# Performance work log

Measured on AMD Instinct MI355X. Metric: run time of the kernel, lower is better.

The kernel has to match this reference:

```python
import jax, jax.numpy as jnp
import numpy as np

KH, KW = 3, 3
STRIDE, PAD, DIL = 1, 1, 1


def setup_inputs() -> dict:
    key = jax.random.key(0)
    k1, k2, k3 = jax.random.split(key, 3)
    B, C, H, W, O = 8, 128, 64, 64, 128
    x = jax.random.normal(k1, (B, C, H, W), jnp.float32)
    # offset layout: [B, 2*K, Ho, Wo], pairs (dy, dx) per kernel tap
    offset = jax.random.normal(k2, (B, 2 * KH * KW, H, W), jnp.float32)
    n = C * KH * KW
    stdv = 1.0 / np.sqrt(n)
    weight = jax.random.uniform(k3, (O, C, KH, KW), jnp.float32, -stdv, stdv)
    bias = jnp.zeros((O,), jnp.float32)
    return {"x": x, "offset": offset, "weight": weight, "bias": bias}


def _deform_conv(x, offset, weight, bias):
    B, C, H, W = x.shape
    O = weight.shape[0]
    K = KH * KW
    Ho = (H + 2 * PAD - DIL * (KH - 1) - 1) // STRIDE + 1
    Wo = (W + 2 * PAD - DIL * (KW - 1) - 1) // STRIDE + 1

    off = offset.reshape(B, K, 2, Ho, Wo)  # (dy, dx) per tap

    # base sampling grid for each kernel tap: [K, Ho, Wo]
    hs = jnp.arange(Ho, dtype=jnp.float32) * STRIDE - PAD
    ws = jnp.arange(Wo, dtype=jnp.float32) * STRIDE - PAD
    ki = jnp.arange(KH, dtype=jnp.float32) * DIL
    kj = jnp.arange(KW, dtype=jnp.float32) * DIL
    base_y = (ki[:, None, None, None] + hs[None, None, :, None])  # [KH,1,Ho,1]
    base_x = (kj[None, :, None, None] + ws[None, None, None, :])  # [1,KW,1,Wo]
    base_y = jnp.broadcast_to(base_y, (KH, KW, Ho, Wo)).reshape(K, Ho, Wo)
    base_x = jnp.broadcast_to(base_x, (KH, KW, Ho, Wo)).reshape(K, Ho, Wo)

    py = base_y[None] + off[:, :, 0]  # [B,K,Ho,Wo]
    px = base_x[None] + off[:, :, 1]

    y0 = jnp.floor(py)
    x0 = jnp.floor(px)
    ly = py - y0  # fractional parts
    lx = px - x0
    y0i = y0.astype(jnp.int32)
    x0i = x0.astype(jnp.int32)

    flat = x.reshape(B, C, H * W)

    def gather(yi, xi, w):
        # zero outside the image (DCN zero-padding semantics)
        valid = (yi >= 0) & (yi < H) & (xi >= 0) & (xi < W)
        idx = jnp.clip(yi, 0, H - 1) * W + jnp.clip(xi, 0, W - 1)  # [B,K,Ho,Wo]
        g = jnp.take_along_axis(flat, idx.reshape(B, 1, -1), axis=2)
        g = g.reshape(B, C, K, Ho, Wo)
        wmask = (w * valid.astype(x.dtype))[:, None]  # [B,1,K,Ho,Wo]
        return g * wmask

    # bilinear accumulation over 4 corners -> im2col columns [B,C,K,Ho,Wo]
    cols = gather(y0i, x0i, (1 - ly) * (1 - lx))
    cols = cols + gather(y0i, x0i + 1, (1 - ly) * lx)
    cols = cols + gather(y0i + 1, x0i, ly * (1 - lx))
    cols = cols + gather(y0i + 1, x0i + 1, ly * lx)

    out = jnp.einsum('ock,bckhw->bohw', weight.reshape(O, C, K), cols)
    return out + bias[None, :, None, None]


def reference(x, offset, weight, bias):
    return _deform_conv(x, offset, weight, bias)
```

## Files before the change

### kernel.cpp

```cpp
#include <hip/hip_runtime.h>


#define BB 8
#define CC 128
#define HH 64
#define WW 64
#define OO 128
#define KTAPS 9

typedef __attribute__((ext_vector_type(8))) short bf16x8;
typedef __attribute__((ext_vector_type(4))) float f32x4;

__device__ __forceinline__ unsigned short f2bf(float f) {
    unsigned u = __float_as_uint(f);
    u += 0x7FFFu + ((u >> 16) & 1u);
    return (unsigned short)(u >> 16);
}
#if __has_builtin(__builtin_amdgcn_cvt_pk_bf16_f32)
typedef __attribute__((ext_vector_type(2))) __bf16 bf16x2_t;
__device__ __forceinline__ unsigned pack2bf(float lo, float hi) {
    bf16x2_t v = __builtin_amdgcn_cvt_pk_bf16_f32(lo, hi);
    unsigned r;
    __builtin_memcpy(&r, &v, 4);
    return r;
}
#else
__device__ __forceinline__ unsigned pack2bf(float lo, float hi) {
    return (unsigned)f2bf(lo) | ((unsigned)f2bf(hi) << 16);
}
#endif
__device__ __forceinline__ float bflo(unsigned p) { return __uint_as_float(p << 16); }
__device__ __forceinline__ float bfhi(unsigned p) { return __uint_as_float(p & 0xFFFF0000u); }

__global__ __launch_bounds__(256)
void prep_kernel(const float* __restrict__ x, const float* __restrict__ wgt,
                 unsigned short* __restrict__ xt, unsigned short* __restrict__ wpk) {
    const int t = threadIdx.x;
    if (blockIdx.x < 512) {
        __shared__ float tile[WW * 132];
        const int b = blockIdx.x >> 6;
        const int h = blockIdx.x & 63;
        const float* src = x + ((size_t)b * CC * HH + h) * WW;
        {
            const int wq = t & 15;
            const int cb = t >> 4;
#pragma unroll
            for (int it = 0; it < 8; ++it) {
                const int c = it * 16 + cb;
                const float4 v = *reinterpret_cast<const float4*>(src + (size_t)c * (HH * WW) + wq * 4);
                tile[(wq * 4 + 0) * 132 + c] = v.x;
                tile[(wq * 4 + 1) * 132 + c] = v.y;
                tile[(wq * 4 + 2) * 132 + c] = v.z;
                tile[(wq * 4 + 3) * 132 + c] = v.w;
            }
        }
        __syncthreads();
        unsigned short* dst = xt + ((size_t)b * HH + h) * WW * CC;
        {
            const int cg = t & 15;
            const int wb = t >> 4;
#pragma unroll
            for (int it = 0; it < 4; ++it) {
                const int w = it * 16 + wb;
                const float* tp = &tile[w * 132 + cg * 8];
                uint4 p;
                p.x = pack2bf(tp[0], tp[1]);
                p.y = pack2bf(tp[2], tp[3]);
                p.z = pack2bf(tp[4], tp[5]);
                p.w = pack2bf(tp[6], tp[7]);
                *reinterpret_cast<uint4*>(&dst[(size_t)w * CC + cg * 8]) = p;
            }
        }
    } else {
        const int id   = (blockIdx.x - 512) * 256 + t;
        const int lane = id & 63;
        const int frag = id >> 6;
        const int nt   = frag & 7;
        const int c0q  = (frag >> 3) & 3;
        const int tap  = frag >> 5;
        const int o    = (nt << 4) + (lane & 15);
        const int c    = (c0q << 5) + ((lane >> 4) << 3);
        const float* s = wgt + ((size_t)o * CC + c) * KTAPS + tap;
        unsigned u[4];
#pragma unroll
        for (int j = 0; j < 4; ++j)
            u[j] = pack2bf(s[(2 * j) * KTAPS], s[(2 * j + 1) * KTAPS]);
        *reinterpret_cast<uint4*>(wpk + (size_t)frag * 512 + lane * 8) =
            make_uint4(u[0], u[1], u[2], u[3]);
    }
}

__global__ __launch_bounds__(256, 4)
void dcn_mfma_kernel(const unsigned short* __restrict__ xt,
                     const unsigned short* __restrict__ wpk,
                     const float* __restrict__ offset,
                     const float* __restrict__ bias,
                     float* __restrict__ out) {
    __shared__ __align__(16) float2 sLL[KTAPS * 32];
    __shared__ __align__(16) short2 sYX[KTAPS * 32];
    __shared__ __align__(16) float  dumpf[2 * 2048];
    __shared__ __align__(16) float  transf[2 * 2560];

    const int t   = threadIdx.x;
    const int bid = blockIdx.x;
    const int b   = bid >> 7;
    const int ho  = (bid >> 1) & 63;
    const int woh = bid & 1;

    for (int s = t; s < KTAPS * 32; s += 256) {
        const int k   = s >> 5;
        const int wol = s & 31;
        const int wo  = (woh << 5) + wol;
        const int ki  = k / 3;
        const int kj  = k - ki * 3;
        const float dy = offset[(((size_t)b * 18 + 2 * k    ) * 64 + ho) * 64 + wo];
        const float dx = offset[(((size_t)b * 18 + 2 * k + 1) * 64 + ho) * 64 + wo];
        const float py = (float)(ho - 1 + ki) + dy;
        const float px = (float)(wo - 1 + kj) + dx;
        const float y0f = floorf(py);
        const float x0f = floorf(px);
        sLL[s] = make_float2(py - y0f, px - x0f);
        sYX[s] = make_short2((short)(int)y0f, (short)(int)x0f);
    }
    __syncthreads();

    f32x4 acc[8];
#pragma unroll
    for (int nt = 0; nt < 8; ++nt) acc[nt] = (f32x4){0.f, 0.f, 0.f, 0.f};

    const int lane = t & 63;
    const int wave = t >> 6;
    const int mi   = wave & 1;
    const int kh   = wave >> 1;
    const int lm   = lane & 15;
    const int quad = lane >> 4;
    const char* xb = (const char*)(xt + (size_t)b * HH * WW * CC);
    const char* wb = (const char*)wpk;
    const int cbase  = (kh << 7) + (quad << 4);
    const int lane16 = lane * 16;

    for (int tap = 0; tap < KTAPS; ++tap) {
        const int rec = (tap << 5) + (mi << 4) + lm;
        const float2 ll = sLL[rec];
        const short2 yx = sYX[rec];
        const int y0 = yx.x, x0 = yx.y;
        const int y1 = y0 + 1, x1 = x0 + 1;
        const float ly = ll.x, lx = ll.y;
        const bool vy0 = ((unsigned)y0 < (unsigned)HH);
        const bool vy1 = ((unsigned)y1 < (unsigned)HH);
        const bool vx0 = ((unsigned)x0 < (unsigned)WW);
        const bool vx1 = ((unsigned)x1 < (unsigned)WW);
        const float w00 = (vy0 && vx0) ? (1.f - ly) * (1.f - lx) : 0.f;
        const float w01 = (vy0 && vx1) ? (1.f - ly) * lx         : 0.f;
        const float w10 = (vy1 && vx0) ? ly * (1.f - lx)         : 0.f;
        const float w11 = (vy1 && vx1) ? ly * lx                 : 0.f;
        const int cy0 = min(max(y0, 0), HH - 1);
        const int cy1 = min(max(y1, 0), HH - 1);
        const int cx0 = min(max(x0, 0), WW - 1);
        const int cx1 = min(max(x1, 0), WW - 1);
        const char* base00 = xb + ((((cy0 << 6) + cx0) << 8) + cbase);
        const char* base01 = xb + ((((cy0 << 6) + cx1) << 8) + cbase);
        const char* base10 = xb + ((((cy1 << 6) + cx0) << 8) + cbase);
        const char* base11 = xb + ((((cy1 << 6) + cx1) << 8) + cbase);

        uint4 a00 = *reinterpret_cast<const uint4*>(base00);
        uint4 a01 = *reinterpret_cast<const uint4*>(base01);
        uint4 a10 = *reinterpret_cast<const uint4*>(base10);
        uint4 a11 = *reinterpret_cast<const uint4*>(base11);

        const char* wtap = wb + ((((tap << 2) + (kh << 1)) << 13)) + lane16;

#pragma unroll
        for (int j = 0; j < 2; ++j) {
            uint4 bfr[8];
            const char* wrow = wtap + (j << 13);
#pragma unroll
            for (int nt = 0; nt < 8; ++nt)
                bfr[nt] = *reinterpret_cast<const uint4*>(wrow + (nt << 10));

            uint4 n00, n01, n10, n11;
            if (j == 0) {
                n00 = *reinterpret_cast<const uint4*>(base00 + 64);
                n01 = *reinterpret_cast<const uint4*>(base01 + 64);
                n10 = *reinterpret_cast<const uint4*>(base10 + 64);
                n11 = *reinterpret_cast<const uint4*>(base11 + 64);
            }

            const unsigned* u00 = reinterpret_cast<const unsigned*>(&a00);
            const unsigned* u01 = reinterpret_cast<const unsigned*>(&a01);
            const unsigned* u10 = reinterpret_cast<const unsigned*>(&a10);
            const unsigned* u11 = reinterpret_cast<const unsigned*>(&a11);
            unsigned afu[4];
#pragma unroll
            for (int jj = 0; jj < 4; ++jj) {
                const float rl = w00 * bflo(u00[jj]) + w01 * bflo(u01[jj])
                               + w10 * bflo(u10[jj]) + w11 * bflo(u11[jj]);
                const float rh = w00 * bfhi(u00[jj]) + w01 * bfhi(u01[jj])
                               + w10 * bfhi(u10[jj]) + w11 * bfhi(u11[jj]);
                afu[jj] = pack2bf(rl, rh);
            }
            bf16x8 afrag;
            __builtin_memcpy(&afrag, afu, 16);
#pragma unroll
            for (int nt = 0; nt < 8; ++nt) {
                bf16x8 bfrag;
                __builtin_memcpy(&bfrag, &bfr[nt], 16);
                acc[nt] = __builtin_amdgcn_mfma_f32_16x16x32_bf16(afrag, bfrag, acc[nt], 0, 0, 0);
            }
            if (j == 0) { a00 = n00; a01 = n01; a10 = n10; a11 = n11; }
        }
    }

    if (kh == 1) {
        float* d = dumpf + mi * 2048;
#pragma unroll
        for (int nt = 0; nt < 8; ++nt)
            *reinterpret_cast<float4*>(&d[((nt << 6) + lane) << 2]) =
                make_float4(acc[nt][0], acc[nt][1], acc[nt][2], acc[nt][3]);
    }
    __syncthreads();
    if (kh == 0) {
        const float* d = dumpf + mi * 2048;
#pragma unroll
        for (int nt = 0; nt < 8; ++nt) {
            const float4 p = *reinterpret_cast<const float4*>(&d[((nt << 6) + lane) << 2]);
            acc[nt][0] += p.x; acc[nt][1] += p.y; acc[nt][2] += p.z; acc[nt][3] += p.w;
        }
        float* scr = transf + mi * 2560;
#pragma unroll
        for (int nt = 0; nt < 8; ++nt) {
            const int o_l = (nt << 4) + lm;
            *reinterpret_cast<float4*>(&scr[o_l * 20 + (quad << 2)]) =
                make_float4(acc[nt][0], acc[nt][1], acc[nt][2], acc[nt][3]);
        }
#pragma unroll
        for (int h = 0; h < 2; ++h) {
            const int o = (h << 6) + lane;
            const float bv = bias[o];
            float* op = out + (((size_t)(b * OO + o) * HH + ho) << 6) + (woh << 5) + (mi << 4);
            const float* sr = scr + o * 20;
#pragma unroll
            for (int jj = 0; jj < 4; ++jj) {
                const float4 f = *reinterpret_cast<const float4*>(sr + jj * 4);
                *reinterpret_cast<float4*>(op + jj * 4) =
                    make_float4(f.x + bv, f.y + bv, f.z + bv, f.w + bv);
            }
        }
    }
}

extern "C" void kernel_launch(void* const* d_in, const int* in_sizes, int n_in,
                              void* d_out, int out_size, void* d_ws, size_t ws_size,
                              hipStream_t stream) {
    const float* x      = (const float*)d_in[0];
    const float* offset = (const float*)d_in[1];
    const float* wgt    = (const float*)d_in[2];
    const float* bias   = (const float*)d_in[3];
    float* out = (float*)d_out;

    unsigned short* xt  = (unsigned short*)d_ws;
    unsigned short* wpk = xt + (size_t)BB * HH * WW * CC;

    hipLaunchKernelGGL(prep_kernel, dim3(512 + 72), dim3(256), 0, stream, x, wgt, xt, wpk);
    hipLaunchKernelGGL(dcn_mfma_kernel, dim3(BB * HH * 2), dim3(256), 0, stream,
                       xt, wpk, offset, bias, out);
}
```

Before: 144.4 us.

## Split deformable-conv blocks into 128-thread tiles of 16 pixels

Result: faster. 140.4 us (-2.8%).

```diff
diff --git a/kernel.cpp b/kernel.cpp
--- a/kernel.cpp
+++ b/kernel.cpp
@@ -90,27 +90,28 @@
     }
 }
 
-__global__ __launch_bounds__(256, 4)
+__global__ __launch_bounds__(128)
 void dcn_mfma_kernel(const unsigned short* __restrict__ xt,
                      const unsigned short* __restrict__ wpk,
                      const float* __restrict__ offset,
                      const float* __restrict__ bias,
                      float* __restrict__ out) {
-    __shared__ __align__(16) float2 sLL[KTAPS * 32];
-    __shared__ __align__(16) short2 sYX[KTAPS * 32];
-    __shared__ __align__(16) float  dumpf[2 * 2048];
-    __shared__ __align__(16) float  transf[2 * 2560];
+    __shared__ __align__(16) float2 sLL[KTAPS * 16];
+    __shared__ __align__(16) short2 sYX[KTAPS * 16];
+    __shared__ __align__(16) float  scr[OO * 21];
 
     const int t   = threadIdx.x;
     const int bid = blockIdx.x;
-    const int b   = bid >> 7;
-    const int ho  = (bid >> 1) & 63;
-    const int woh = bid & 1;
-
-    for (int s = t; s < KTAPS * 32; s += 256) {
-        const int k   = s >> 5;
-        const int wol = s & 31;
-        const int wo  = (woh << 5) + wol;
+    const int b   = bid & 7;
+    const int s   = bid >> 3;
+    const int ho  = s >> 2;
+    const int mt  = s & 3;
+    const int wobase = mt << 4;
+
+    for (int r = t; r < KTAPS * 16; r += 128) {
+        const int k   = r >> 4;
+        const int wol = r & 15;
+        const int wo  = wobase + wol;
         const int ki  = k / 3;
         const int kj  = k - ki * 3;
         const float dy = offset[(((size_t)b * 18 + 2 * k    ) * 64 + ho) * 64 + wo];
@@ -119,8 +120,8 @@
         const float px = (float)(wo - 1 + kj) + dx;
         const float y0f = floorf(py);
         const float x0f = floorf(px);
-        sLL[s] = make_float2(py - y0f, px - x0f);
-        sYX[s] = make_short2((short)(int)y0f, (short)(int)x0f);
+        sLL[r] = make_float2(py - y0f, px - x0f);
+        sYX[r] = make_short2((short)(int)y0f, (short)(int)x0f);
     }
     __syncthreads();
 
@@ -129,18 +130,16 @@
     for (int nt = 0; nt < 8; ++nt) acc[nt] = (f32x4){0.f, 0.f, 0.f, 0.f};
 
     const int lane = t & 63;
-    const int wave = t >> 6;
-    const int mi   = wave & 1;
-    const int kh   = wave >> 1;
+    const int kh   = t >> 6;
     const int lm   = lane & 15;
     const int quad = lane >> 4;
-    const char* xb = (const char*)(xt + (size_t)b * HH * WW * CC);
+    const char* xb = (const char*)xt + ((size_t)b << 20);
     const char* wb = (const char*)wpk;
     const int cbase  = (kh << 7) + (quad << 4);
-    const int lane16 = lane * 16;
+    const int lane16 = lane << 4;
 
     for (int tap = 0; tap < KTAPS; ++tap) {
-        const int rec = (tap << 5) + (mi << 4) + lm;
+        const int rec = (tap << 4) + lm;
         const float2 ll = sLL[rec];
         const short2 yx = sYX[rec];
         const int y0 = yx.x, x0 = yx.y;
@@ -168,7 +167,7 @@
         uint4 a10 = *reinterpret_cast<const uint4*>(base10);
         uint4 a11 = *reinterpret_cast<const uint4*>(base11);
 
-        const char* wtap = wb + ((((tap << 2) + (kh << 1)) << 13)) + lane16;
+        const char* wtap = wb + (tap << 15) + (kh << 14) + lane16;
 
 #pragma unroll
         for (int j = 0; j < 2; ++j) {
@@ -212,39 +211,33 @@
     }
 
     if (kh == 1) {
-        float* d = dumpf + mi * 2048;
 #pragma unroll
         for (int nt = 0; nt < 8; ++nt)
-            *reinterpret_cast<float4*>(&d[((nt << 6) + lane) << 2]) =
+            *reinterpret_cast<float4*>(&scr[((nt << 4) + lm) * 21 + (quad << 2)]) =
                 make_float4(acc[nt][0], acc[nt][1], acc[nt][2], acc[nt][3]);
     }
     __syncthreads();
     if (kh == 0) {
-        const float* d = dumpf + mi * 2048;
 #pragma unroll
         for (int nt = 0; nt < 8; ++nt) {
-            const float4 p = *reinterpret_cast<const float4*>(&d[((nt << 6) + lane) << 2]);
-            acc[nt][0] += p.x; acc[nt][1] += p.y; acc[nt][2] += p.z; acc[nt][3] += p.w;
-        }
-        float* scr = transf + mi * 2560;
-#pragma unroll
-        for (int nt = 0; nt < 8; ++nt) {
-            const int o_l = (nt << 4) + lm;
-            *reinterpret_cast<float4*>(&scr[o_l * 20 + (quad << 2)]) =
-                make_float4(acc[nt][0], acc[nt][1], acc[nt][2], acc[nt][3]);
-        }
-#pragma unroll
-        for (int h = 0; h < 2; ++h) {
-            const int o = (h << 6) + lane;
-            const float bv = bias[o];
-            float* op = out + (((size_t)(b * OO + o) * HH + ho) << 6) + (woh << 5) + (mi << 4);
-            const float* sr = scr + o * 20;
-#pragma unroll
-            for (int jj = 0; jj < 4; ++jj) {
-                const float4 f = *reinterpret_cast<const float4*>(sr + jj * 4);
-                *reinterpret_cast<float4*>(op + jj * 4) =
-                    make_float4(f.x + bv, f.y + bv, f.z + bv, f.w + bv);
-            }
+            float* p = &scr[((nt << 4) + lm) * 21 + (quad << 2)];
+            const float4 v = *reinterpret_cast<const float4*>(p);
+            *reinterpret_cast<float4*>(p) =
+                make_float4(v.x + acc[nt][0], v.y + acc[nt][1],
+                            v.z + acc[nt][2], v.w + acc[nt][3]);
+        }
+    }
+    __syncthreads();
+    {
+        const int o  = (kh << 6) + lane;
+        const float bv = bias[o];
+        float* op = out + (((size_t)(b * OO + o) * HH + ho) << 6) + wobase;
+        const float* sr = scr + o * 21;
+#pragma unroll
+        for (int jj = 0; jj < 4; ++jj) {
+            const float4 f = *reinterpret_cast<const float4*>(sr + jj * 4);
+            *reinterpret_cast<float4*>(op + jj * 4) =
+                make_float4(f.x + bv, f.y + bv, f.z + bv, f.w + bv);
         }
     }
 }
@@ -262,6 +255,6 @@
     unsigned short* wpk = xt + (size_t)BB * HH * WW * CC;
 
     hipLaunchKernelGGL(prep_kernel, dim3(512 + 72), dim3(256), 0, stream, x, wgt, xt, wpk);
-    hipLaunchKernelGGL(dcn_mfma_kernel, dim3(BB * HH * 2), dim3(256), 0, stream,
+    hipLaunchKernelGGL(dcn_mfma_kernel, dim3(BB * HH * 4 * 2 / 2), dim3(128), 0, stream,
                        xt, wpk, offset, bias, out);
 }
```
